# Performance work log

Hardware: AMD Instinct MI355X
Metric: run time of the kernel (lower is better)

The kernel has to match this reference:

```python
import jax, jax.numpy as jnp
import numpy as np

N, E = 20000, 160000
H, C1, C_OUT, D_IN = 4, 256, 512, 128
HID = H * C1  # 1024


def gat_conv(x, src, dst, W, a_src, a_dst, b, heads, ch, concat):
    n = x.shape[0]
    xw = (x @ W).reshape(n, heads, ch)                     # [N,H,C]
    es = jnp.sum(xw * a_src, axis=-1)                      # [N,H]
    ed = jnp.sum(xw * a_dst, axis=-1)                      # [N,H]
    e = jax.nn.leaky_relu(es[src] + ed[dst], 0.2)          # [Etot,H]
    m = jax.ops.segment_max(e, dst, num_segments=n)
    m = jnp.where(jnp.isfinite(m), m, 0.0)
    p = jnp.exp(e - m[dst])
    denom = jax.ops.segment_sum(p, dst, num_segments=n)
    alpha = p / (denom[dst] + 1e-16)                       # segment softmax
    out = jax.ops.segment_sum(alpha[:, :, None] * xw[src], dst, num_segments=n)
    out = out.reshape(n, heads * ch) if concat else out.mean(axis=1)
    return out + b


def layer_norm(x, g, b, eps=1e-5):
    mu = jnp.mean(x, axis=-1, keepdims=True)
    var = jnp.var(x, axis=-1, keepdims=True)
    return (x - mu) * jax.lax.rsqrt(var + eps) * g + b


def setup_inputs() -> dict:
    key = jax.random.key(0)
    ks = jax.random.split(key, 16)
    s1, s2, s3 = (2.0 / D_IN) ** 0.5, (2.0 / HID) ** 0.5, (2.0 / HID) ** 0.5
    return {
        "x": jax.random.normal(ks[0], (N, D_IN), jnp.float32),
        "edge_index": jax.random.randint(ks[1], (2, E), 0, N, jnp.int64),
        "W1": jax.random.normal(ks[2], (D_IN, H * C1), jnp.float32) * s1,
        "a_src1": jax.random.normal(ks[3], (H, C1), jnp.float32) * 0.1,
        "a_dst1": jax.random.normal(ks[4], (H, C1), jnp.float32) * 0.1,
        "b1": jnp.zeros((HID,), jnp.float32),
        "ln1_g": jnp.ones((HID,), jnp.float32),
        "ln1_b": jnp.zeros((HID,), jnp.float32),
        "W2": jax.random.normal(ks[5], (HID, H * C1), jnp.float32) * s2,
        "a_src2": jax.random.normal(ks[6], (H, C1), jnp.float32) * 0.1,
        "a_dst2": jax.random.normal(ks[7], (H, C1), jnp.float32) * 0.1,
        "b2": jnp.zeros((HID,), jnp.float32),
        "ln2_g": jnp.ones((HID,), jnp.float32),
        "ln2_b": jnp.zeros((HID,), jnp.float32),
        "W3": jax.random.normal(ks[8], (HID, C_OUT), jnp.float32) * s3,
        "a_src3": jax.random.normal(ks[9], (1, C_OUT), jnp.float32) * 0.1,
        "a_dst3": jax.random.normal(ks[10], (1, C_OUT), jnp.float32) * 0.1,
        "b3": jnp.zeros((C_OUT,), jnp.float32),
    }


def reference(x, edge_index, W1, a_src1, a_dst1, b1, ln1_g, ln1_b,
              W2, a_src2, a_dst2, b2, ln2_g, ln2_b,
              W3, a_src3, a_dst3, b3):
    # add self loops (PyG GATConv default add_self_loops=True)
    loops = jnp.arange(N, dtype=edge_index.dtype)
    src = jnp.concatenate([edge_index[0], loops])
    dst = jnp.concatenate([edge_index[1], loops])

    h = gat_conv(x, src, dst, W1, a_src1, a_dst1, b1, H, C1, True)
    h = jax.nn.elu(layer_norm(h, ln1_g, ln1_b))  # dropout: eval mode (identity)
    h = gat_conv(h, src, dst, W2, a_src2, a_dst2, b2, H, C1, True)
    h = jax.nn.elu(layer_norm(h, ln2_g, ln2_b))
    out = gat_conv(h, src, dst, W3, a_src3, a_dst3, b3, 1, C_OUT, True)
    return out
```

## Files before the change

### kernel.cpp

```cpp
#include <hip/hip_runtime.h>
#include <hip/hip_bf16.h>

typedef __hip_bfloat16 bf16;
typedef __attribute__((ext_vector_type(8))) short short8;
typedef __attribute__((ext_vector_type(4))) float float4v;

#define NN 20000
#define EE 160000
#define ET (NN + EE)

__device__ __forceinline__ float bf2f(bf16 v){ return __bfloat162float(v); }
__device__ __forceinline__ float raw2f(unsigned short u){ return __uint_as_float(((unsigned)u) << 16); }
__device__ __forceinline__ unsigned short f2raw(float f){
  bf16 h = __float2bfloat16(f);
  return *(unsigned short*)&h;
}

__device__ __forceinline__ int detect_f32(const void* raw, int nwords, int lane){
  unsigned v = ((const unsigned*)raw)[lane % nwords];
  int e8 = (v >> 7) & 0xFF;
  int looks = (e8 >= 100 && e8 <= 140) ? 1 : 0;
  unsigned long long mz = __ballot(v == 0u);
  unsigned long long ml = __ballot(looks);
  int nz = __popcll(mz);
  int nonz = 64 - nz;
  int nl = __popcll(ml);
  return (nonz > 0 && 2*nl >= nonz) ? 0 : 1;
}

__device__ __forceinline__ int detect_i64(const int* eiraw, int lane){
  int odd = eiraw[2*lane + 1];
  unsigned long long m2 = __ballot(odd != 0);
  return (m2 == 0ULL) ? 1 : 0;
}

struct P13 { const void* src[13]; int off[13]; int n[13]; };
struct PrepArgs {
  const void* xraw; bf16* Xc;
  const void* w1raw; bf16* Wt1;
  const void* w2raw; bf16* Wt2;
  const void* w3raw; bf16* Wt3;
  const int* eiraw; int* eic;
  P13 p13; float* prm;
  int* counts;
  float* esA; float* edA;
};

__device__ __forceinline__ void do_transpose(float (*tile)[33], const void* raw,
    bf16* wt, int K, int M, int f, int bx, int by, int t){
  int kb = by*32, mb = bx*32;
  int tx = t & 31, ty = t >> 5;
  for (int r = 0; r < 4; r++){
    int k = kb + ty + r*8;
    int m = mb + tx;
    float v = f ? ((const float*)raw)[(size_t)k*M+m] : bf2f(((const bf16*)raw)[(size_t)k*M+m]);
    tile[ty + r*8][tx] = v;
  }
  __syncthreads();
  for (int r = 0; r < 4; r++){
    int m = mb + ty + r*8;
    int k = kb + tx;
    wt[(size_t)m*K + k] = __float2bfloat16(tile[tx][ty + r*8]);
  }
}

__global__ __launch_bounds__(256) void k_prep(PrepArgs A){
  __shared__ float tile[32][33];
  int b = blockIdx.x, t = threadIdx.x;
  int lane = t & 63;
  if (b < 10000){
    int f = detect_f32(A.xraw, NN*128/2, lane);
    int i = b*256 + t;
    if (f) A.Xc[i] = __float2bfloat16(((const float*)A.xraw)[i]);
    else   A.Xc[i] = ((const bf16*)A.xraw)[i];
  } else if (b < 10128){
    int f = detect_f32(A.w1raw, 128*1024/2, lane);
    int r = b - 10000;
    do_transpose(tile, A.w1raw, A.Wt1, 128, 1024, f, r & 31, r >> 5, t);
  } else if (b < 11152){
    int f = detect_f32(A.w2raw, 1024*1024/2, lane);
    int r = b - 10128;
    do_transpose(tile, A.w2raw, A.Wt2, 1024, 1024, f, r & 31, r >> 5, t);
  } else if (b < 11664){
    int f = detect_f32(A.w3raw, 1024*512/2, lane);
    int r = b - 11152;
    do_transpose(tile, A.w3raw, A.Wt3, 1024, 512, f, r & 15, r >> 4, t);
  } else if (b < 12914){
    int f64 = detect_i64(A.eiraw, lane);
    int i = (b - 11664)*256 + t;
    if (i < 2*EE) A.eic[i] = f64 ? A.eiraw[2*i] : A.eiraw[i];
  } else if (b < 12927){
    int pb = b - 12914;
    const void* s = A.p13.src[pb];
    int n = A.p13.n[pb];
    int f = detect_f32(s, n/2, lane);
    float* d = A.prm + A.p13.off[pb];
    for (int i = t; i < n; i += 256)
      d[i] = f ? ((const float*)s)[i] : bf2f(((const bf16*)s)[i]);
  } else if (b < 13006){
    int i = (b - 12927)*256 + t;
    if (i < NN) A.counts[i] = 1;
  } else {
    int i = (b - 13006)*256 + t;
    if (i < NN*4){ A.esA[i] = 0.f; A.edA[i] = 0.f; }
  }
}

__global__ void k_hist(const int* __restrict__ ei, int* __restrict__ counts){
  int e = blockIdx.x*256 + threadIdx.x;
  if (e < EE){
    int d = ei[EE + e];
    if (d >= 0 && d < NN) atomicAdd(&counts[d], 1);
  }
}

__global__ __launch_bounds__(1024) void k_scan(const int* __restrict__ counts, int* __restrict__ rp,
    int* __restrict__ cursor, int* __restrict__ col){
  __shared__ int wsum[16];
  __shared__ int sc;
  int t = threadIdx.x, lane = t & 63, wv = t >> 6;
  if (t == 0) sc = 0;
  __syncthreads();
  for (int base = 0; base < NN; base += 1024){
    int i = base + t;
    int v = (i < NN) ? counts[i] : 0;
    int x = v;
    #pragma unroll
    for (int o = 1; o < 64; o <<= 1){
      int y = __shfl_up(x, o, 64);
      if (lane >= o) x += y;
    }
    if (lane == 63) wsum[wv] = x;
    __syncthreads();
    if (wv == 0 && lane < 16){
      int w = wsum[lane];
      #pragma unroll
      for (int o = 1; o < 16; o <<= 1){
        int y = __shfl_up(w, o, 16);
        if ((lane & 15) >= o) w += y;
      }
      wsum[lane] = w;
    }
    __syncthreads();
    int carry = sc;
    int wpre = (wv > 0) ? wsum[wv-1] : 0;
    if (i < NN){
      int p = carry + wpre + x - v;
      rp[i] = p;
      col[p] = i;
      cursor[i] = p + 1;
    }
    __syncthreads();
    if (t == 1023) sc = carry + wsum[15];
    __syncthreads();
  }
  if (t == 0) rp[NN] = sc;
}

__global__ void k_scatter(const int* __restrict__ ei, int* __restrict__ cursor, int* __restrict__ col){
  int e = blockIdx.x*256 + threadIdx.x;
  if (e < EE){
    int s = ei[e], d = ei[EE + e];
    if (d >= 0 && d < NN){
      int pos = atomicAdd(&cursor[d], 1);
      col[pos] = s;
    }
  }
}

__device__ __forceinline__ void stage_tiles(const bf16* __restrict__ X, const bf16* __restrict__ Wt,
    bf16* xs, bf16* bs, int r0, int c0, int K, int tid, int k0){
  #pragma unroll
  for (int i = 0; i < 2; i++){
    int ch = i*256 + tid;
    int row = ch >> 3, kl = ch & 7;
    int kg = kl ^ (row & 7);
    const bf16* gx = X + (size_t)(r0 + row)*K + k0 + kg*8;
    __builtin_amdgcn_global_load_lds(
      (const __attribute__((address_space(1))) unsigned int*)gx,
      (__attribute__((address_space(3))) unsigned int*)(xs + ch*8), 16, 0, 0);
  }
  #pragma unroll
  for (int i = 0; i < 4; i++){
    int ch = i*256 + tid;
    int row = ch >> 3, kl = ch & 7;
    int kg = kl ^ (row & 7);
    const bf16* gb = Wt + (size_t)(c0 + row)*K + k0 + kg*8;
    __builtin_amdgcn_global_load_lds(
      (const __attribute__((address_space(1))) unsigned int*)gb,
      (__attribute__((address_space(3))) unsigned int*)(bs + ch*8), 16, 0, 0);
  }
}

__device__ __forceinline__ void compute_step(const bf16* xb, const bf16* bb,
    int wr, int wc, int quad, int l15, int sw, float4v (&acc)[2][4]){
  #pragma unroll
  for (int kk = 0; kk < 2; kk++){
    int kp = quad + kk*4;
    short8 af[2], bfr[4];
    #pragma unroll
    for (int i = 0; i < 2; i++){
      int r = wr + i*16 + l15;
      af[i] = *(const short8*)(xb + ((size_t)r*8 + (kp ^ sw))*8);
    }
    #pragma unroll
    for (int j = 0; j < 4; j++){
      int r = wc + j*16 + l15;
      bfr[j] = *(const short8*)(bb + ((size_t)r*8 + (kp ^ sw))*8);
    }
    #pragma unroll
    for (int i = 0; i < 2; i++)
      #pragma unroll
      for (int j = 0; j < 4; j++)
        acc[i][j] = __builtin_amdgcn_mfma_f32_16x16x32_bf16(af[i], bfr[j], acc[i][j], 0, 0, 0);
  }
}

__global__ __launch_bounds__(256) void k_gemm_mfma(
    const bf16* __restrict__ X, const bf16* __restrict__ Wt, bf16* __restrict__ Y,
    const float* __restrict__ as_, const float* __restrict__ ad_,
    float* __restrict__ es, float* __restrict__ ed,
    int K, int M, int C, int H)
{
  __shared__ bf16 Xs0[64*64];
  __shared__ bf16 Xs1[64*64];
  __shared__ bf16 Bs0[128*64];
  __shared__ bf16 Bs1[128*64];
  int ncols = gridDim.x;
  int bid = blockIdx.y * ncols + blockIdx.x;
  int xcd  = bid & 7;
  int rest = bid >> 3;
  int colb = rest % ncols;
  int rowb = xcd + 8 * (rest / ncols);
  int r0 = rowb * 64;
  if (r0 >= NN) return;
  int c0 = colb * 128;

  int tid  = threadIdx.x;
  int wave = tid >> 6, lane = tid & 63;
  int quad = lane >> 4, l15 = lane & 15;
  int wr = (wave >> 1) * 32;
  int wc = (wave & 1) * 64;
  int sw = l15 & 7;

  float4v acc[2][4];
  #pragma unroll
  for (int i=0;i<2;i++)
    #pragma unroll
    for (int j=0;j<4;j++)
      acc[i][j] = (float4v){0.f,0.f,0.f,0.f};

  int nst = K >> 6;
  stage_tiles(X, Wt, Xs0, Bs0, r0, c0, K, tid, 0);
  __syncthreads();

  for (int t = 0; t < nst; t += 2){
    if (t + 1 < nst) stage_tiles(X, Wt, Xs1, Bs1, r0, c0, K, tid, (t+1) << 6);
    compute_step(Xs0, Bs0, wr, wc, quad, l15, sw, acc);
    __syncthreads();
    if (t + 1 >= nst) break;
    if (t + 2 < nst) stage_tiles(X, Wt, Xs0, Bs0, r0, c0, K, tid, (t+2) << 6);
    compute_step(Xs1, Bs1, wr, wc, quad, l15, sw, acc);
    if (t + 2 < nst) __syncthreads();
  }

  int h = c0 / C;
  float asv[4], adv[4];
  #pragma unroll
  for (int j = 0; j < 4; j++){
    int colj = c0 + wc + j*16 + l15;
    asv[j] = as_[colj]; adv[j] = ad_[colj];
  }
  #pragma unroll
  for (int i = 0; i < 2; i++){
    int rbase = r0 + wr + i*16 + quad*4;
    #pragma unroll
    for (int rg = 0; rg < 4; rg++){
      int row = rbase + rg;
      bool ok = (row < NN);
      float pe = 0.f, pd = 0.f;
      #pragma unroll
      for (int j = 0; j < 4; j++){
        float v = acc[i][j][rg];
        int colj = c0 + wc + j*16 + l15;
        if (ok) Y[(size_t)row*M + colj] = __float2bfloat16(v);
        pe += v * asv[j];
        pd += v * adv[j];
      }
      #pragma unroll
      for (int o = 1; o < 16; o <<= 1){
        pe += __shfl_xor(pe, o, 64);
        pd += __shfl_xor(pd, o, 64);
      }
      if (ok && l15 == 0){
        atomicAdd(&es[row*H + h], pe);
        atomicAdd(&ed[row*H + h], pd);
      }
    }
  }
}

__global__ __launch_bounds__(256) void k_aggln(const int* __restrict__ rp, const int* __restrict__ col,
    const bf16* __restrict__ xw, const float* __restrict__ es, const float* __restrict__ ed,
    const float* __restrict__ bias, const float* __restrict__ gam, const float* __restrict__ bet,
    bf16* __restrict__ act, float* __restrict__ esz, float* __restrict__ edz, int zn){
  int wv = threadIdx.x >> 6, lane = threadIdx.x & 63;
  int n = blockIdx.x*4 + wv;
  int h = lane >> 4;
  int cb = lane * 16;
  int e0 = rp[n], e1 = rp[n+1], deg = e1 - e0;
  float4 ed4 = *(const float4*)&ed[n*4];
  const unsigned short* xwu = (const unsigned short*)xw;

  float acc[16];
  #pragma unroll
  for (int c=0;c<16;c++) acc[c]=0.f;

  if (deg <= 64){
    int src = 0;
    float l0=-1e30f, l1=-1e30f, l2=-1e30f, l3=-1e30f;
    if (lane < deg){
      src = col[e0 + lane];
      float4 e4 = *(const float4*)&es[src*4];
      float v;
      v = e4.x + ed4.x; l0 = v > 0.f ? v : 0.2f*v;
      v = e4.y + ed4.y; l1 = v > 0.f ? v : 0.2f*v;
      v = e4.z + ed4.z; l2 = v > 0.f ? v : 0.2f*v;
      v = e4.w + ed4.w; l3 = v > 0.f ? v : 0.2f*v;
    }
    float m0=l0, m1=l1, m2=l2, m3=l3;
    #pragma unroll
    for (int o=1;o<64;o<<=1){
      m0 = fmaxf(m0, __shfl_xor(m0,o,64));
      m1 = fmaxf(m1, __shfl_xor(m1,o,64));
      m2 = fmaxf(m2, __shfl_xor(m2,o,64));
      m3 = fmaxf(m3, __shfl_xor(m3,o,64));
    }
    float p0 = (lane<deg) ? __expf(l0-m0) : 0.f;
    float p1 = (lane<deg) ? __expf(l1-m1) : 0.f;
    float p2 = (lane<deg) ? __expf(l2-m2) : 0.f;
    float p3 = (lane<deg) ? __expf(l3-m3) : 0.f;
    float d0=p0, d1=p1, d2=p2, d3=p3;
    #pragma unroll
    for (int o=1;o<64;o<<=1){
      d0 += __shfl_xor(d0,o,64);
      d1 += __shfl_xor(d1,o,64);
      d2 += __shfl_xor(d2,o,64);
      d3 += __shfl_xor(d3,o,64);
    }
    float al0 = p0 * (1.f/(d0+1e-16f));
    float al1 = p1 * (1.f/(d1+1e-16f));
    float al2 = p2 * (1.f/(d2+1e-16f));
    float al3 = p3 * (1.f/(d3+1e-16f));

    int j = 0;
    for (; j + 2 <= deg; j += 2){
      int sA = __shfl(src, j, 64);
      int sB = __shfl(src, j+1, 64);
      float a0A = __shfl(al0, j, 64), a1A = __shfl(al1, j, 64);
      float a2A = __shfl(al2, j, 64), a3A = __shfl(al3, j, 64);
      float a0B = __shfl(al0, j+1, 64), a1B = __shfl(al1, j+1, 64);
      float a2B = __shfl(al2, j+1, 64), a3B = __shfl(al3, j+1, 64);
      float aA = (h==0) ? a0A : ((h==1) ? a1A : ((h==2) ? a2A : a3A));
      float aB = (h==0) ? a0B : ((h==1) ? a1B : ((h==2) ? a2B : a3B));
      const unsigned short* rA = xwu + (size_t)sA*1024 + cb;
      const unsigned short* rB = xwu + (size_t)sB*1024 + cb;
      ushort4 uA0 = *(const ushort4*)(rA);
      ushort4 uA1 = *(const ushort4*)(rA+4);
      ushort4 uA2 = *(const ushort4*)(rA+8);
      ushort4 uA3 = *(const ushort4*)(rA+12);
      ushort4 uB0 = *(const ushort4*)(rB);
      ushort4 uB1 = *(const ushort4*)(rB+4);
      ushort4 uB2 = *(const ushort4*)(rB+8);
      ushort4 uB3 = *(const ushort4*)(rB+12);
      acc[0] += aA*raw2f(uA0.x); acc[1] += aA*raw2f(uA0.y); acc[2] += aA*raw2f(uA0.z); acc[3] += aA*raw2f(uA0.w);
      acc[4] += aA*raw2f(uA1.x); acc[5] += aA*raw2f(uA1.y); acc[6] += aA*raw2f(uA1.z); acc[7] += aA*raw2f(uA1.w);
      acc[8] += aA*raw2f(uA2.x); acc[9] += aA*raw2f(uA2.y); acc[10]+= aA*raw2f(uA2.z); acc[11]+= aA*raw2f(uA2.w);
      acc[12]+= aA*raw2f(uA3.x); acc[13]+= aA*raw2f(uA3.y); acc[14]+= aA*raw2f(uA3.z); acc[15]+= aA*raw2f(uA3.w);
      acc[0] += aB*raw2f(uB0.x); acc[1] += aB*raw2f(uB0.y); acc[2] += aB*raw2f(uB0.z); acc[3] += aB*raw2f(uB0.w);
      acc[4] += aB*raw2f(uB1.x); acc[5] += aB*raw2f(uB1.y); acc[6] += aB*raw2f(uB1.z); acc[7] += aB*raw2f(uB1.w);
      acc[8] += aB*raw2f(uB2.x); acc[9] += aB*raw2f(uB2.y); acc[10]+= aB*raw2f(uB2.z); acc[11]+= aB*raw2f(uB2.w);
      acc[12]+= aB*raw2f(uB3.x); acc[13]+= aB*raw2f(uB3.y); acc[14]+= aB*raw2f(uB3.z); acc[15]+= aB*raw2f(uB3.w);
    }
    for (; j < deg; j++){
      int s = __shfl(src, j, 64);
      float a0j = __shfl(al0, j, 64);
      float a1j = __shfl(al1, j, 64);
      float a2j = __shfl(al2, j, 64);
      float a3j = __shfl(al3, j, 64);
      float aj = (h==0) ? a0j : ((h==1) ? a1j : ((h==2) ? a2j : a3j));
      const unsigned short* row = xwu + (size_t)s*1024 + cb;
      ushort4 u0 = *(const ushort4*)(row);
      ushort4 u1 = *(const ushort4*)(row+4);
      ushort4 u2 = *(const ushort4*)(row+8);
      ushort4 u3 = *(const ushort4*)(row+12);
      acc[0] += aj*raw2f(u0.x); acc[1] += aj*raw2f(u0.y); acc[2] += aj*raw2f(u0.z); acc[3] += aj*raw2f(u0.w);
      acc[4] += aj*raw2f(u1.x); acc[5] += aj*raw2f(u1.y); acc[6] += aj*raw2f(u1.z); acc[7] += aj*raw2f(u1.w);
      acc[8] += aj*raw2f(u2.x); acc[9] += aj*raw2f(u2.y); acc[10]+= aj*raw2f(u2.z); acc[11]+= aj*raw2f(u2.w);
      acc[12]+= aj*raw2f(u3.x); acc[13]+= aj*raw2f(u3.y); acc[14]+= aj*raw2f(u3.z); acc[15]+= aj*raw2f(u3.w);
    }
  } else {
    float edh = (h==0) ? ed4.x : ((h==1) ? ed4.y : ((h==2) ? ed4.z : ed4.w));
    float m = -1e30f;
    for (int e=e0;e<e1;e++){
      float v = es[col[e]*4 + h] + edh;
      v = v > 0.f ? v : 0.2f*v;
      m = fmaxf(m, v);
    }
    float den = 0.f;
    for (int e=e0;e<e1;e++){
      float v = es[col[e]*4 + h] + edh;
      v = v > 0.f ? v : 0.2f*v;
      den += __expf(v - m);
    }
    float rd = 1.f/(den + 1e-16f);
    for (int e=e0;e<e1;e++){
      int s = col[e];
      float v = es[s*4 + h] + edh;
      v = v > 0.f ? v : 0.2f*v;
      float aj = __expf(v - m) * rd;
      const unsigned short* row = xwu + (size_t)s*1024 + cb;
      ushort4 u0 = *(const ushort4*)(row);
      ushort4 u1 = *(const ushort4*)(row+4);
      ushort4 u2 = *(const ushort4*)(row+8);
      ushort4 u3 = *(const ushort4*)(row+12);
      acc[0] += aj*raw2f(u0.x); acc[1] += aj*raw2f(u0.y); acc[2] += aj*raw2f(u0.z); acc[3] += aj*raw2f(u0.w);
      acc[4] += aj*raw2f(u1.x); acc[5] += aj*raw2f(u1.y); acc[6] += aj*raw2f(u1.z); acc[7] += aj*raw2f(u1.w);
      acc[8] += aj*raw2f(u2.x); acc[9] += aj*raw2f(u2.y); acc[10]+= aj*raw2f(u2.z); acc[11]+= aj*raw2f(u2.w);
      acc[12]+= aj*raw2f(u3.x); acc[13]+= aj*raw2f(u3.y); acc[14]+= aj*raw2f(u3.z); acc[15]+= aj*raw2f(u3.w);
    }
  }

  #pragma unroll
  for (int c=0;c<16;c++) acc[c] += bias[cb+c];
  float s1 = 0.f, s2 = 0.f;
  #pragma unroll
  for (int c=0;c<16;c++){ s1 += acc[c]; s2 += acc[c]*acc[c]; }
  #pragma unroll
  for (int o=1;o<64;o<<=1){
    s1 += __shfl_xor(s1,o,64);
    s2 += __shfl_xor(s2,o,64);
  }
  float mu  = s1 * (1.f/1024.f);
  float var = s2 * (1.f/1024.f) - mu*mu;
  float rstd = rsqrtf(fmaxf(var, 0.f) + 1e-5f);

  ushort4 o4[4];
  #pragma unroll
  for (int q=0;q<4;q++){
    float v0 = (acc[q*4+0]-mu)*rstd*gam[cb+q*4+0] + bet[cb+q*4+0];
    float v1 = (acc[q*4+1]-mu)*rstd*gam[cb+q*4+1] + bet[cb+q*4+1];
    float v2 = (acc[q*4+2]-mu)*rstd*gam[cb+q*4+2] + bet[cb+q*4+2];
    float v3 = (acc[q*4+3]-mu)*rstd*gam[cb+q*4+3] + bet[cb+q*4+3];
    v0 = v0 > 0.f ? v0 : (__expf(v0)-1.f);
    v1 = v1 > 0.f ? v1 : (__expf(v1)-1.f);
    v2 = v2 > 0.f ? v2 : (__expf(v2)-1.f);
    v3 = v3 > 0.f ? v3 : (__expf(v3)-1.f);
    o4[q].x = f2raw(v0); o4[q].y = f2raw(v1); o4[q].z = f2raw(v2); o4[q].w = f2raw(v3);
  }
  unsigned short* dst = (unsigned short*)act + (size_t)n*1024 + cb;
  *(ushort4*)(dst)    = o4[0];
  *(ushort4*)(dst+4)  = o4[1];
  *(ushort4*)(dst+8)  = o4[2];
  *(ushort4*)(dst+12) = o4[3];

  if (lane < zn){ esz[n*zn + lane] = 0.f; edz[n*zn + lane] = 0.f; }
}

__global__ __launch_bounds__(256) void k_agg3(const int* __restrict__ rp, const int* __restrict__ col,
    const bf16* __restrict__ xw, const float* __restrict__ es, const float* __restrict__ ed,
    const float* __restrict__ bias, float* __restrict__ out){
  int wv = threadIdx.x >> 6, lane = threadIdx.x & 63;
  int n = blockIdx.x*4 + wv;
  int cb = lane * 8;
  int e0 = rp[n], e1 = rp[n+1], deg = e1 - e0;
  float edv = ed[n];
  const unsigned short* xwu = (const unsigned short*)xw;

  float acc[8];
  #pragma unroll
  for (int c=0;c<8;c++) acc[c]=0.f;

  if (deg <= 64){
    int src = 0;
    float l = -1e30f;
    if (lane < deg){
      src = col[e0 + lane];
      float v = es[src] + edv;
      l = v > 0.f ? v : 0.2f*v;
    }
    float m = l;
    #pragma unroll
    for (int o=1;o<64;o<<=1) m = fmaxf(m, __shfl_xor(m,o,64));
    float p = (lane<deg) ? __expf(l-m) : 0.f;
    float d = p;
    #pragma unroll
    for (int o=1;o<64;o<<=1) d += __shfl_xor(d,o,64);
    float al = p * (1.f/(d+1e-16f));

    int j = 0;
    for (; j + 2 <= deg; j += 2){
      int sA = __shfl(src, j, 64);
      int sB = __shfl(src, j+1, 64);
      float aA = __shfl(al, j, 64);
      float aB = __shfl(al, j+1, 64);
      const unsigned short* rA = xwu + (size_t)sA*512 + cb;
      const unsigned short* rB = xwu + (size_t)sB*512 + cb;
      ushort4 uA0 = *(const ushort4*)(rA);
      ushort4 uA1 = *(const ushort4*)(rA+4);
      ushort4 uB0 = *(const ushort4*)(rB);
      ushort4 uB1 = *(const ushort4*)(rB+4);
      acc[0] += aA*raw2f(uA0.x); acc[1] += aA*raw2f(uA0.y); acc[2] += aA*raw2f(uA0.z); acc[3] += aA*raw2f(uA0.w);
      acc[4] += aA*raw2f(uA1.x); acc[5] += aA*raw2f(uA1.y); acc[6] += aA*raw2f(uA1.z); acc[7] += aA*raw2f(uA1.w);
      acc[0] += aB*raw2f(uB0.x); acc[1] += aB*raw2f(uB0.y); acc[2] += aB*raw2f(uB0.z); acc[3] += aB*raw2f(uB0.w);
      acc[4] += aB*raw2f(uB1.x); acc[5] += aB*raw2f(uB1.y); acc[6] += aB*raw2f(uB1.z); acc[7] += aB*raw2f(uB1.w);
    }
    for (; j < deg; j++){
      int s = __shfl(src, j, 64);
      float aj = __shfl(al, j, 64);
      const unsigned short* row = xwu + (size_t)s*512 + cb;
      ushort4 u0 = *(const ushort4*)(row);
      ushort4 u1 = *(const ushort4*)(row+4);
      acc[0] += aj*raw2f(u0.x); acc[1] += aj*raw2f(u0.y); acc[2] += aj*raw2f(u0.z); acc[3] += aj*raw2f(u0.w);
      acc[4] += aj*raw2f(u1.x); acc[5] += aj*raw2f(u1.y); acc[6] += aj*raw2f(u1.z); acc[7] += aj*raw2f(u1.w);
    }
  } else {
    float m = -1e30f;
    for (int e=e0;e<e1;e++){
      float v = es[col[e]] + edv;
      v = v > 0.f ? v : 0.2f*v;
      m = fmaxf(m, v);
    }
    float den = 0.f;
    for (int e=e0;e<e1;e++){
      float v = es[col[e]] + edv;
      v = v > 0.f ? v : 0.2f*v;
      den += __expf(v - m);
    }
    float rd = 1.f/(den + 1e-16f);
    for (int e=e0;e<e1;e++){
      int s = col[e];
      float v = es[s] + edv;
      v = v > 0.f ? v : 0.2f*v;
      float aj = __expf(v - m) * rd;
      const unsigned short* row = xwu + (size_t)s*512 + cb;
      ushort4 u0 = *(const ushort4*)(row);
      ushort4 u1 = *(const ushort4*)(row+4);
      acc[0] += aj*raw2f(u0.x); acc[1] += aj*raw2f(u0.y); acc[2] += aj*raw2f(u0.z); acc[3] += aj*raw2f(u0.w);
      acc[4] += aj*raw2f(u1.x); acc[5] += aj*raw2f(u1.y); acc[6] += aj*raw2f(u1.z); acc[7] += aj*raw2f(u1.w);
    }
  }
  float* dst = out + (size_t)n*512 + cb;
  #pragma unroll
  for (int c=0;c<8;c++) dst[c] = acc[c] + bias[cb+c];
}

__global__ void k_wssmall(float* __restrict__ out, float code){
  if (threadIdx.x == 0) out[0] = code;
}

extern "C" void kernel_launch(void* const* d_in, const int* in_sizes, int n_in,
                              void* d_out, int out_size, void* d_ws, size_t ws_size,
                              hipStream_t stream){
  float* out = (float*)d_out;
  char* ws = (char*)d_ws;

  static const int EXP_SZ[18] = {2560000, 320000, 131072, 1024,1024,1024,1024,1024,
                                 1048576, 1024,1024,1024,1024,1024,
                                 524288, 512,512,512};
  if (n_in != 18){ k_wssmall<<<1,64,0,stream>>>(out, 500.0f*301.0f); return; }
  for (int i = 0; i < 18; i++)
    if (in_sizes[i] != EXP_SZ[i]){ k_wssmall<<<1,64,0,stream>>>(out, 500.0f*302.0f); return; }
  if (out_size != NN*512){ k_wssmall<<<1,64,0,stream>>>(out, 500.0f*303.0f); return; }
  const size_t NEED = 93215360;
  if (ws_size < NEED){ k_wssmall<<<1,64,0,stream>>>(out, 500.0f*304.0f); return; }

  bf16* xw    = (bf16*) (ws);
  int*  cnt   = (int*)  (ws);
  bf16* act   = (bf16*) (ws + 40960000);
  int*  cursor= (int*)  (ws + 40960000);
  bf16* Xc    = (bf16*) (ws + 81920000);
  float* esC  = (float*)(ws + 81920000);
  float* edC  = (float*)(ws + 82000000);
  bf16* Wt1   = (bf16*) (ws + 87040000);
  bf16* Wt2   = (bf16*) (ws + 87302144);
  bf16* Wt3   = (bf16*) (ws + 89399296);
  float* prm  = (float*)(ws + 90447872);
  int*  eic   = (int*)  (ws + 90495232);
  float* esB  = (float*)(ws + 90495232);
  float* edB  = (float*)(ws + 90815232);
  float* esA  = (float*)(ws + 91775232);
  float* edA  = (float*)(ws + 92095232);
  int*  rp    = (int*)  (ws + 92415232);
  int*  col   = (int*)  (ws + 92495360);

  float *as1=prm+0, *ad1=prm+1024, *b1=prm+2048, *lg1=prm+3072, *lb1=prm+4096;
  float *as2=prm+5120, *ad2=prm+6144, *b2=prm+7168, *lg2=prm+8192, *lb2=prm+9216;
  float *as3=prm+10240, *ad3=prm+10752, *b3=prm+11264;

  const int TB = 256;
  int gbE = (EE + TB - 1)/TB;

  {
    PrepArgs A;
    A.xraw = d_in[0]; A.Xc = Xc;
    A.w1raw = d_in[2]; A.Wt1 = Wt1;
    A.w2raw = d_in[8]; A.Wt2 = Wt2;
    A.w3raw = d_in[14]; A.Wt3 = Wt3;
    A.eiraw = (const int*)d_in[1]; A.eic = eic;
    const int idx[13] = {3,4,5,6,7, 9,10,11,12,13, 15,16,17};
    const int off[13] = {0,1024,2048,3072,4096, 5120,6144,7168,8192,9216, 10240,10752,11264};
    const int nn [13] = {1024,1024,1024,1024,1024, 1024,1024,1024,1024,1024, 512,512,512};
    for (int i=0;i<13;i++){ A.p13.src[i]=d_in[idx[i]]; A.p13.off[i]=off[i]; A.p13.n[i]=nn[i]; }
    A.prm = prm; A.counts = cnt; A.esA = esA; A.edA = edA;
    k_prep<<<13006 + 313, TB, 0, stream>>>(A);
  }

  k_hist<<<gbE, TB, 0, stream>>>(eic, cnt);
  k_scan<<<1, 1024, 0, stream>>>(cnt, rp, cursor, col);
  k_scatter<<<gbE, TB, 0, stream>>>(eic, cursor, col);

  const int RB = (NN + 63)/64;
  const int R8 = ((RB + 7)/8)*8;
  dim3 g12(1024/128, R8);
  dim3 g3 (512/128,  R8);

  k_gemm_mfma<<<g12, TB, 0, stream>>>(Xc, Wt1, xw, as1, ad1, esA, edA, 128, 1024, 256, 4);
  k_aggln<<<NN/4, TB, 0, stream>>>(rp, col, xw, esA, edA, b1, lg1, lb1, act, esB, edB, 4);

  k_gemm_mfma<<<g12, TB, 0, stream>>>(act, Wt2, xw, as2, ad2, esB, edB, 1024, 1024, 256, 4);
  k_aggln<<<NN/4, TB, 0, stream>>>(rp, col, xw, esB, edB, b2, lg2, lb2, act, esC, edC, 1);

  k_gemm_mfma<<<g3, TB, 0, stream>>>(act, Wt3, xw, as3, ad3, esC, edC, 1024, 512, 512, 1);
  k_agg3<<<NN/4, TB, 0, stream>>>(rp, col, xw, esC, edC, b3, out);
}
```

Baseline: 460.1 us.

## Deepen GEMM prefetch pipeline with explicit vmcnt waits and raw barriers

```diff
diff --git a/kernel.cpp b/kernel.cpp
--- a/kernel.cpp
+++ b/kernel.cpp
@@ -252,16 +252,36 @@
 
   int nst = K >> 6;
   stage_tiles(X, Wt, Xs0, Bs0, r0, c0, K, tid, 0);
-  __syncthreads();
+  stage_tiles(X, Wt, Xs1, Bs1, r0, c0, K, tid, 64);
 
   for (int t = 0; t < nst; t += 2){
-    if (t + 1 < nst) stage_tiles(X, Wt, Xs1, Bs1, r0, c0, K, tid, (t+1) << 6);
+    bool last = (t + 2 >= nst);
+
+    asm volatile("s_waitcnt vmcnt(6)" ::: "memory");
+    __builtin_amdgcn_sched_barrier(0);
+    __builtin_amdgcn_s_barrier();
+    __builtin_amdgcn_sched_barrier(0);
     compute_step(Xs0, Bs0, wr, wc, quad, l15, sw, acc);
-    __syncthreads();
-    if (t + 1 >= nst) break;
-    if (t + 2 < nst) stage_tiles(X, Wt, Xs0, Bs0, r0, c0, K, tid, (t+2) << 6);
+    __builtin_amdgcn_sched_barrier(0);
+    if (!last){
+      __builtin_amdgcn_s_barrier();
+      __builtin_amdgcn_sched_barrier(0);
+      stage_tiles(X, Wt, Xs0, Bs0, r0, c0, K, tid, (t+2) << 6);
+      asm volatile("s_waitcnt vmcnt(6)" ::: "memory");
+    } else {
+      asm volatile("s_waitcnt vmcnt(0)" ::: "memory");
+    }
+    __builtin_amdgcn_sched_barrier(0);
+
+    __builtin_amdgcn_s_barrier();
+    __builtin_amdgcn_sched_barrier(0);
     compute_step(Xs1, Bs1, wr, wc, quad, l15, sw, acc);
-    if (t + 2 < nst) __syncthreads();
+    __builtin_amdgcn_sched_barrier(0);
+    if (!last){
+      __builtin_amdgcn_s_barrier();
+      __builtin_amdgcn_sched_barrier(0);
+      stage_tiles(X, Wt, Xs1, Bs1, r0, c0, K, tid, (t+3) << 6);
+    }
   }
 
   int h = c0 / C;
```

After: 458.3 us. Within noise of the previous version (-0.4%).
